# Optimization experiments

Measured on AMD Instinct MI355X. Metric: run time of the kernel, lower is better.

## Reference

```python
import jax, jax.numpy as jnp
import numpy as np

B, H, W, DIM = 16, 64, 64, 256
EXPAND = 2
D_INNER = DIM * EXPAND      # 512
HID = D_INNER // 2          # 256 per GRU direction


def setup_inputs() -> dict:
    ks = jax.random.split(jax.random.key(0), 10)
    g = lambda i, shape, s=0.05: jax.random.normal(ks[i], shape, dtype=jnp.float32) * s
    return {
        "x": jax.random.normal(ks[0], (B, H, W, DIM), dtype=jnp.float32),
        "ln_gamma": jnp.ones((DIM,), jnp.float32),
        "ln_beta": jnp.zeros((DIM,), jnp.float32),
        "mlp_w1": g(1, (32, 4), 0.3),
        "mlp_b1": jnp.zeros((32,), jnp.float32),
        "mlp_w2": g(2, (4, 32), 0.3),
        "mlp_b2": jnp.zeros((4,), jnp.float32),
        "in_w": g(3, (D_INNER, DIM)),
        "in_b": jnp.zeros((D_INNER,), jnp.float32),
        "gru_wih_f": g(4, (3 * HID, D_INNER)),
        "gru_whh_f": g(5, (3 * HID, HID)),
        "gru_bih_f": jnp.zeros((3 * HID,), jnp.float32),
        "gru_bhh_f": jnp.zeros((3 * HID,), jnp.float32),
        "gru_wih_b": g(6, (3 * HID, D_INNER)),
        "gru_whh_b": g(7, (3 * HID, HID)),
        "gru_bih_b": jnp.zeros((3 * HID,), jnp.float32),
        "gru_bhh_b": jnp.zeros((3 * HID,), jnp.float32),
        "out_w": g(8, (DIM, D_INNER)),
        "out_b": jnp.zeros((DIM,), jnp.float32),
    }


def _resize_linear_axis(x, out_size, axis):
    """torch F.interpolate(mode='bilinear', align_corners=False) along one axis
    (the other axis has scale 1 -> identity, so 1-D resize is exact)."""
    in_size = x.shape[axis]
    scale = in_size / out_size
    src = (jnp.arange(out_size, dtype=jnp.float32) + 0.5) * scale - 0.5
    src = jnp.clip(src, 0.0, in_size - 1)
    i0 = jnp.floor(src).astype(jnp.int32)
    i1 = jnp.minimum(i0 + 1, in_size - 1)
    w = (src - i0.astype(jnp.float32))
    x0 = jnp.take(x, i0, axis=axis)
    x1 = jnp.take(x, i1, axis=axis)
    shape = [1] * x.ndim
    shape[axis] = out_size
    w = w.reshape(shape)
    return x0 * (1.0 - w) + x1 * w


def _avgpool3_mean(g):
    """F.avg_pool2d(g, 3, stride=1, padding=1) (count_include_pad=True), then
    spatial mean -> [B, 1]."""
    s = jax.lax.reduce_window(g, 0.0, jax.lax.add, (1, 1, 3, 3), (1, 1, 1, 1),
                              [(0, 0), (0, 0), (1, 1), (1, 1)])
    return (s / 9.0).mean(axis=(2, 3))


def _gru_dir(xp, whh, bhh, reverse):
    """One GRU direction. xp: [B, L, 3h] precomputed input-side gates."""
    hid = whh.shape[1]
    h0 = jnp.zeros((xp.shape[0], hid), xp.dtype)

    def step(h, xt):
        gh = h @ whh.T + bhh
        xr, xz, xn = jnp.split(xt, 3, axis=-1)
        hr, hz, hn = jnp.split(gh, 3, axis=-1)
        r = jax.nn.sigmoid(xr + hr)
        z = jax.nn.sigmoid(xz + hz)
        n = jnp.tanh(xn + r * hn)
        h_new = (1.0 - z) * n + z * h
        return h_new, h_new

    _, ys = jax.lax.scan(step, h0, jnp.swapaxes(xp, 0, 1), reverse=reverse)
    return jnp.swapaxes(ys, 0, 1)  # [B, L, h], ys[t] aligned with input t


def _forward(x, ln_gamma, ln_beta, mlp_w1, mlp_b1, mlp_w2, mlp_b2,
             in_w, in_b, gru_wih_f, gru_whh_f, gru_bih_f, gru_bhh_f,
             gru_wih_b, gru_whh_b, gru_bih_b, gru_bhh_b, out_w, out_b):
    Bx, Hx, Wx, C = x.shape
    # LayerNorm over channels
    mu = x.mean(-1, keepdims=True)
    var = ((x - mu) ** 2).mean(-1, keepdims=True)
    xn = (x - mu) / jnp.sqrt(var + 1e-5) * ln_gamma + ln_beta

    # --- GradientDirectionSelector ---
    gray = xn.mean(-1)[:, None]                                   # [B,1,H,W]
    gp = jnp.pad(gray, ((0, 0), (0, 0), (1, 1), (1, 1)), mode="reflect")
    grad_h = jnp.abs(gp[:, :, :, 2:] - gp[:, :, :, :-2])          # [B,1,H+2,W]
    grad_v = jnp.abs(gp[:, :, 2:, :] - gp[:, :, :-2, :])          # [B,1,H,W+2]
    grad_h = _resize_linear_axis(grad_h, Hx, axis=2)              # [B,1,H,W]
    grad_v = _resize_linear_axis(grad_v, Wx, axis=3)              # [B,1,H,W]
    grad_d = (grad_h + grad_v) * 0.5
    grad_a = jnp.abs(grad_h - grad_v)
    scores = jnp.concatenate(
        [_avgpool3_mean(g) for g in (grad_h, grad_v, grad_d, grad_a)], axis=1)  # [B,4]
    h1 = jax.nn.relu(scores @ mlp_w1.T + mlp_b1)
    logits = h1 @ mlp_w2.T + mlp_b2
    probs = jax.nn.softmax(logits, axis=-1)
    idx = jnp.argmax(probs, axis=-1)  # topk=1 indices, [B]

    # --- direction-routed scan (dir 1 -> vertical transpose; 0/2/3 -> row-major) ---
    seq_h = xn.reshape(Bx, Hx * Wx, C)
    seq_v = jnp.swapaxes(xn, 1, 2).reshape(Bx, Hx * Wx, C)
    seq = jnp.where((idx == 1)[:, None, None], seq_v, seq_h)      # [B,L,C]

    # --- FastSequenceBlock: in_proj -> biGRU -> out_proj ---
    z = seq @ in_w.T + in_b                                       # [B,L,d_inner]
    yf = _gru_dir(z @ gru_wih_f.T + gru_bih_f, gru_whh_f, gru_bhh_f, False)
    yb = _gru_dir(z @ gru_wih_b.T + gru_bih_b, gru_whh_b, gru_bhh_b, True)
    y = jnp.concatenate([yf, yb], axis=-1) @ out_w.T + out_b      # [B,L,C]

    # unscan (row-major reshape, as in the original) + residual
    return x + y.reshape(Bx, Hx, Wx, C)


def reference(x, ln_gamma, ln_beta, mlp_w1, mlp_b1, mlp_w2, mlp_b2,
              in_w, in_b, gru_wih_f, gru_whh_f, gru_bih_f, gru_bhh_f,
              gru_wih_b, gru_whh_b, gru_bih_b, gru_bhh_b, out_w, out_b):
    return _forward(x, ln_gamma, ln_beta, mlp_w1, mlp_b1, mlp_w2, mlp_b2,
                    in_w, in_b, gru_wih_f, gru_whh_f, gru_bih_f, gru_bhh_f,
                    gru_wih_b, gru_whh_b, gru_bih_b, gru_bhh_b, out_w, out_b)
```

## Files before the change

kernel.cpp:

```cpp
#include <hip/hip_runtime.h>


#define L_   4096
#define CH   32
#define NCH  128

typedef __attribute__((ext_vector_type(8))) _Float16 half8;
typedef __attribute__((ext_vector_type(2))) _Float16 half2v;
typedef __attribute__((ext_vector_type(4))) float f32x4;

__device__ __forceinline__ unsigned short f2h(float f) {
  _Float16 h = (_Float16)f;
  return __builtin_bit_cast(unsigned short, h);
}
__device__ __forceinline__ float h2f(unsigned short u) {
  return (float)__builtin_bit_cast(_Float16, u);
}
__device__ __forceinline__ float sigm(float x) {
  return __builtin_amdgcn_rcpf(1.f + __expf(-x));
}
__device__ __forceinline__ float tanhf_(float x) {
  return 1.f - 2.f * __builtin_amdgcn_rcpf(1.f + __expf(2.f * x));
}
__device__ __forceinline__ float dot2(unsigned w, unsigned h, float c) {
  return __builtin_amdgcn_fdot2(__builtin_bit_cast(half2v, w),
                                __builtin_bit_cast(half2v, h), c, false);
}

__global__ __launch_bounds__(256) void k_f2h(const float* __restrict__ in,
                                             unsigned short* __restrict__ out,
                                             int n) {
  int i = blockIdx.x * 256 + threadIdx.x;
  if (i < n) out[i] = f2h(in[i]);
}

__global__ __launch_bounds__(256) void k_wcomb(const float* __restrict__ wih_f,
                                               const float* __restrict__ wih_b,
                                               const float* __restrict__ in_w,
                                               unsigned short* __restrict__ wcomb) {
  const int n = blockIdx.x;
  const float* wrow = (n < 768) ? (wih_f + (long)n * 512)
                                : (wih_b + (long)(n - 768) * 512);
  const int k = threadIdx.x;
  float acc = 0.f;
  for (int j = 0; j < 512; ++j) acc += wrow[j] * in_w[j * 256 + k];
  wcomb[(long)n * 256 + k] = f2h(acc);
}

__global__ __launch_bounds__(256) void k_bcomb(const float* __restrict__ wih_f,
                                               const float* __restrict__ wih_b,
                                               const float* __restrict__ in_b,
                                               const float* __restrict__ bih_f,
                                               const float* __restrict__ bih_b,
                                               const float* __restrict__ bhh_f,
                                               const float* __restrict__ bhh_b,
                                               float* __restrict__ badj) {
  int n = blockIdx.x * 256 + threadIdx.x;
  if (n >= 1536) return;
  const int dir = n >= 768;
  const int g = dir ? (n - 768) : n;
  const float* wrow = (dir ? wih_b : wih_f) + (long)g * 512;
  float acc = (dir ? bih_b : bih_f)[g];
  for (int j = 0; j < 512; ++j) acc += wrow[j] * in_b[j];
  if (g < 512) acc += (dir ? bhh_b : bhh_f)[g];
  badj[n] = acc;
}

__global__ __launch_bounds__(256) void k_ln(const float* __restrict__ x,
                                            const float* __restrict__ gamma,
                                            const float* __restrict__ beta,
                                            unsigned short* __restrict__ xn,
                                            float* __restrict__ gray) {
  const int lane = threadIdx.x & 63;
  const long pix = (long)blockIdx.x * 4 + (threadIdx.x >> 6);
  const float4 v = *(const float4*)(x + pix * 256 + lane * 4);
  float s = v.x + v.y + v.z + v.w;
  float s2 = v.x * v.x + v.y * v.y + v.z * v.z + v.w * v.w;
#pragma unroll
  for (int off = 32; off > 0; off >>= 1) {
    s += __shfl_xor(s, off, 64);
    s2 += __shfl_xor(s2, off, 64);
  }
  const float mu = s * (1.f / 256.f);
  const float var = fmaxf(s2 * (1.f / 256.f) - mu * mu, 0.f);
  const float rstd = rsqrtf(var + 1e-5f);
  const float4 gm = *(const float4*)(gamma + lane * 4);
  const float4 bt = *(const float4*)(beta + lane * 4);
  float o0 = (v.x - mu) * rstd * gm.x + bt.x;
  float o1 = (v.y - mu) * rstd * gm.y + bt.y;
  float o2 = (v.z - mu) * rstd * gm.z + bt.z;
  float o3 = (v.w - mu) * rstd * gm.w + bt.w;
  ushort4 o;
  o.x = f2h(o0); o.y = f2h(o1); o.z = f2h(o2); o.w = f2h(o3);
  *(ushort4*)(xn + pix * 256 + lane * 4) = o;
  float gs = o0 + o1 + o2 + o3;
#pragma unroll
  for (int off = 32; off > 0; off >>= 1) gs += __shfl_xor(gs, off, 64);
  if (lane == 0) gray[pix] = gs * (1.f / 256.f);
}

__device__ __forceinline__ int refl64(int m) {
  return m < 0 ? -m : (m > 63 ? 126 - m : m);
}

__global__ __launch_bounds__(256) void k_sel(const float* __restrict__ gray,
                                             const float* __restrict__ w1,
                                             const float* __restrict__ b1,
                                             const float* __restrict__ w2,
                                             const float* __restrict__ b2,
                                             int* __restrict__ flag) {
  __shared__ float g[64][65];
  __shared__ float part[4][4];
  const int b = blockIdx.x;
  const int tid = threadIdx.x;
  for (int r = 0; r < 16; ++r) {
    int p = tid + 256 * r;
    g[p >> 6][p & 63] = gray[(long)b * 4096 + p];
  }
  __syncthreads();
  const float S = 66.f / 64.f;
  float sh = 0.f, sv = 0.f, sd = 0.f, sa = 0.f;
  for (int rr = 0; rr < 16; ++rr) {
    int p = tid + 256 * rr;
    int h = p >> 6, w = p & 63;
    float srci = (h + 0.5f) * S - 0.5f;
    int i0 = (int)srci;
    float ai = srci - (float)i0;
    int i1 = i0 + 1; if (i1 > 65) i1 = 65;
    int r0 = refl64(i0 - 1), r1 = refl64(i1 - 1);
    int wl = w ? (w - 1) : 1;
    int wr2 = (w == 63) ? 62 : (w + 1);
    float GH0 = fabsf(g[r0][wr2] - g[r0][wl]);
    float GH1 = fabsf(g[r1][wr2] - g[r1][wl]);
    float ghr = GH0 + ai * (GH1 - GH0);
    float srcj = (w + 0.5f) * S - 0.5f;
    int j0 = (int)srcj;
    float aj = srcj - (float)j0;
    int j1 = j0 + 1; if (j1 > 65) j1 = 65;
    int c0 = refl64(j0 - 1), c1 = refl64(j1 - 1);
    int hu = h ? (h - 1) : 1;
    int hd = (h == 63) ? 62 : (h + 1);
    float GV0 = fabsf(g[hd][c0] - g[hu][c0]);
    float GV1 = fabsf(g[hd][c1] - g[hu][c1]);
    float gvr = GV0 + aj * (GV1 - GV0);
    float wt = ((h == 0 || h == 63) ? 2.f : 3.f) *
               ((w == 0 || w == 63) ? 2.f : 3.f);
    sh += wt * ghr;
    sv += wt * gvr;
    sd += wt * 0.5f * (ghr + gvr);
    sa += wt * fabsf(ghr - gvr);
  }
#pragma unroll
  for (int off = 32; off > 0; off >>= 1) {
    sh += __shfl_xor(sh, off, 64);
    sv += __shfl_xor(sv, off, 64);
    sd += __shfl_xor(sd, off, 64);
    sa += __shfl_xor(sa, off, 64);
  }
  if ((tid & 63) == 0) {
    part[tid >> 6][0] = sh; part[tid >> 6][1] = sv;
    part[tid >> 6][2] = sd; part[tid >> 6][3] = sa;
  }
  __syncthreads();
  if (tid == 0) {
    float sc[4];
    for (int k = 0; k < 4; ++k)
      sc[k] = (part[0][k] + part[1][k] + part[2][k] + part[3][k]) * (1.f / 36864.f);
    float logits[4];
    for (int k = 0; k < 4; ++k) logits[k] = b2[k];
    for (int j = 0; j < 32; ++j) {
      float hj = b1[j];
      for (int i = 0; i < 4; ++i) hj += sc[i] * w1[j * 4 + i];
      hj = fmaxf(hj, 0.f);
      for (int k = 0; k < 4; ++k) logits[k] += hj * w2[k * 32 + j];
    }
    int idx = 0;
    float best = logits[0];
    for (int k = 1; k < 4; ++k)
      if (logits[k] > best) { best = logits[k]; idx = k; }
    flag[b] = (idx == 1) ? 1 : 0;
  }
}

__global__ __launch_bounds__(256) void k_gemm(const unsigned short* __restrict__ A,
                                              const unsigned short* __restrict__ Bw,
                                              const float* __restrict__ bias,
                                              const float* __restrict__ resid,
                                              float* __restrict__ out,
                                              int K, int N) {
  __shared__ unsigned short Al[128][40];
  __shared__ unsigned short Bl[128][40];
  const int tid = threadIdx.x;
  const long m0 = (long)blockIdx.x * 128;
  const int n0 = blockIdx.y * 128;
  const int rA = tid >> 2;
  const int cp = (tid & 3) * 8;

  const unsigned short* a0p = A + (m0 + rA) * K + cp;
  const unsigned short* a1p = A + (m0 + rA + 64) * K + cp;
  const unsigned short* b0p = Bw + (long)(n0 + rA) * K + cp;
  const unsigned short* b1p = Bw + (long)(n0 + rA + 64) * K + cp;

  const int wv = tid >> 6, lane = tid & 63;
  const int wm = (wv >> 1) * 64, wn = (wv & 1) * 64;
  const int fr = lane & 15, fq = lane >> 4;

  const f32x4 zero4 = {0.f, 0.f, 0.f, 0.f};
  f32x4 acc[4][4];
#pragma unroll
  for (int i = 0; i < 4; ++i)
#pragma unroll
    for (int j = 0; j < 4; ++j) acc[i][j] = zero4;

  for (int k0 = 0; k0 < K; k0 += 32) {
    half8 va0 = *(const half8*)(a0p + k0);
    half8 va1 = *(const half8*)(a1p + k0);
    half8 vb0 = *(const half8*)(b0p + k0);
    half8 vb1 = *(const half8*)(b1p + k0);
    __syncthreads();
    *(half8*)&Al[rA][cp] = va0;
    *(half8*)&Al[rA + 64][cp] = va1;
    *(half8*)&Bl[rA][cp] = vb0;
    *(half8*)&Bl[rA + 64][cp] = vb1;
    __syncthreads();
    half8 af[4], bf[4];
#pragma unroll
    for (int i = 0; i < 4; ++i) af[i] = *(const half8*)&Al[wm + i * 16 + fr][fq * 8];
#pragma unroll
    for (int j = 0; j < 4; ++j) bf[j] = *(const half8*)&Bl[wn + j * 16 + fr][fq * 8];
#pragma unroll
    for (int i = 0; i < 4; ++i)
#pragma unroll
      for (int j = 0; j < 4; ++j)
        acc[i][j] = __builtin_amdgcn_mfma_f32_16x16x32_f16(af[i], bf[j], acc[i][j], 0, 0, 0);
  }

#pragma unroll
  for (int j = 0; j < 4; ++j) {
    const int col = n0 + wn + j * 16 + fr;
    const float bv = bias[col];
#pragma unroll
    for (int i = 0; i < 4; ++i) {
      const long mbase = m0 + wm + i * 16 + fq * 4;
#pragma unroll
      for (int r = 0; r < 4; ++r) {
        const long m = mbase + r;
        out[m * N + col] = acc[i][j][r] + bv + resid[m * N + col];
      }
    }
  }
}

__global__ __launch_bounds__(768, 3) void k_scan(
    const unsigned short* __restrict__ xn,
    const unsigned short* __restrict__ wcomb,
    const float* __restrict__ badj,
    const unsigned short* __restrict__ whh16,
    const float* __restrict__ bhhf,
    const float* __restrict__ bhhb,
    const int* __restrict__ flag,
    unsigned short* __restrict__ ycat) {
  const int dir = blockIdx.x & 1;
  const int b = blockIdx.x >> 1;
  const unsigned short* whh = whh16 + (long)dir * (768 * 256);
  const float* bhh = dir ? bhhb : bhhf;
  const unsigned short* wcd = wcomb + (long)dir * (768 * 256);
  const float* bcd = badj + dir * 768;
  const int tid = threadIdx.x;
  const int g = tid >> 8;
  const int u = tid & 255;
  const int wv = tid >> 6;
  const int lane = tid & 63;
  const int fr = lane & 15;
  const int fq = lane >> 4;
  const int fb = flag[b];

  __shared__ unsigned short xplds[CH][768];
  __shared__ unsigned short ylds[CH][256];
  __shared__ uint4 hl4[2][32];
  __shared__ float ghlds[512];

  float Bnh = 0.f;
  if (g == 2) Bnh = bhh[512 + u];
  float hreg = 0.f;
  if (tid < 128) ((unsigned*)hl4[0])[tid] = 0;

  const long xnb = (long)b * 4096;
  unsigned short* yb = ycat + (long)b * (L_ * 512) + dir * 256;

  const f32x4 zero4 = {0.f, 0.f, 0.f, 0.f};
  int pb = 0;

  for (int c = 0; c < NCH; ++c) {
    const int cc = dir ? (NCH - 1 - c) : c;
    const int t0 = cc * CH;

    if (c > 0) {
      const int pt0 = (dir ? (NCH - c) : (c - 1)) * CH;
#pragma unroll
      for (int k = 0; k < 2; ++k) {
        const int idx = tid + 768 * k;
        if (idx < 1024) {
          const int tsx = idx >> 5;
          const int cl = (idx & 31) * 8;
          half8 v = *(const half8*)&ylds[tsx][cl];
          *(half8*)(yb + (long)(pt0 + tsx) * 512 + cl) = v;
        }
      }
    }

    {
      const unsigned short* arow0;
      const unsigned short* arow1;
      {
        int t = t0 + fr;
        int p = fb ? (((t & 63) << 6) | (t >> 6)) : t;
        arow0 = xn + (xnb + p) * 256 + fq * 8;
        t = t0 + 16 + fr;
        p = fb ? (((t & 63) << 6) | (t >> 6)) : t;
        arow1 = xn + (xnb + p) * 256 + fq * 8;
      }
      f32x4 acc0[4], acc1[4];
#pragma unroll
      for (int i = 0; i < 4; ++i) { acc0[i] = zero4; acc1[i] = zero4; }
#pragma unroll
      for (int s = 0; s < 8; ++s) {
        half8 a0v = *(const half8*)(arow0 + s * 32);
        half8 a1v = *(const half8*)(arow1 + s * 32);
#pragma unroll
        for (int i = 0; i < 4; ++i) {
          const int n = (wv * 4 + i) * 16 + fr;
          half8 bfr = *(const half8*)(wcd + (long)n * 256 + s * 32 + fq * 8);
          acc0[i] = __builtin_amdgcn_mfma_f32_16x16x32_f16(a0v, bfr, acc0[i], 0, 0, 0);
          acc1[i] = __builtin_amdgcn_mfma_f32_16x16x32_f16(a1v, bfr, acc1[i], 0, 0, 0);
        }
      }
#pragma unroll
      for (int i = 0; i < 4; ++i) {
        const int n = (wv * 4 + i) * 16 + fr;
        const float bv = bcd[n];
#pragma unroll
        for (int r = 0; r < 4; ++r) {
          xplds[fq * 4 + r][n] = f2h(acc0[i][r] + bv);
          xplds[16 + fq * 4 + r][n] = f2h(acc1[i][r] + bv);
        }
      }
    }
    __syncthreads();

    uint4 wq[32];
    {
      const unsigned short* wp = whh + (long)tid * 256;
      asm volatile("" : "+v"(wp));
#pragma unroll
      for (int i = 0; i < 32; ++i) wq[i] = *(const uint4*)(wp + i * 8);
    }

    for (int lt = 0; lt < CH; ++lt) {
      const int ts = dir ? (CH - 1 - lt) : lt;
      const uint4* hp = hl4[pb];
      float a0 = 0.f, a1 = 0.f, a2 = 0.f, a3 = 0.f;
#pragma unroll
      for (int i = 0; i < 32; ++i) {
        uint4 hv = hp[i];
        a0 = dot2(wq[i].x, hv.x, a0);
        a1 = dot2(wq[i].y, hv.y, a1);
        a2 = dot2(wq[i].z, hv.z, a2);
        a3 = dot2(wq[i].w, hv.w, a3);
      }
      const float gh = (a0 + a1) + (a2 + a3);
      if (g == 1) ghlds[u] = h2f(xplds[ts][tid]) + gh;
      else if (g == 2) ghlds[256 + u] = gh + Bnh;
      __syncthreads();
      if (g == 0) {
        const float r = sigm(h2f(xplds[ts][u]) + gh);
        const float z = sigm(ghlds[u]);
        const float n = tanhf_(h2f(xplds[ts][512 + u]) + r * ghlds[256 + u]);
        hreg = n + z * (hreg - n);
        const unsigned short hb = f2h(hreg);
        ((unsigned short*)hl4[pb ^ 1])[u] = hb;
        ylds[ts][u] = hb;
      }
      pb ^= 1;
      __syncthreads();
    }
  }
  {
    const int pt0 = (dir ? 0 : (NCH - 1)) * CH;
#pragma unroll
    for (int k = 0; k < 2; ++k) {
      const int idx = tid + 768 * k;
      if (idx < 1024) {
        const int tsx = idx >> 5;
        const int cl = (idx & 31) * 8;
        half8 v = *(const half8*)&ylds[tsx][cl];
        *(half8*)(yb + (long)(pt0 + tsx) * 512 + cl) = v;
      }
    }
  }
}

extern "C" void kernel_launch(void* const* d_in, const int* in_sizes, int n_in,
                              void* d_out, int out_size, void* d_ws, size_t ws_size,
                              hipStream_t stream) {
  (void)in_sizes; (void)n_in; (void)out_size; (void)ws_size;
  const float* x     = (const float*)d_in[0];
  const float* lng   = (const float*)d_in[1];
  const float* lnb   = (const float*)d_in[2];
  const float* w1    = (const float*)d_in[3];
  const float* b1    = (const float*)d_in[4];
  const float* w2    = (const float*)d_in[5];
  const float* b2    = (const float*)d_in[6];
  const float* in_w  = (const float*)d_in[7];
  const float* in_b  = (const float*)d_in[8];
  const float* wih_f = (const float*)d_in[9];
  const float* whh_f = (const float*)d_in[10];
  const float* bih_f = (const float*)d_in[11];
  const float* bhh_f = (const float*)d_in[12];
  const float* wih_b = (const float*)d_in[13];
  const float* whh_b = (const float*)d_in[14];
  const float* bih_b = (const float*)d_in[15];
  const float* bhh_b = (const float*)d_in[16];
  const float* out_w = (const float*)d_in[17];
  const float* out_b = (const float*)d_in[18];

  char* ws = (char*)d_ws;
  unsigned short* xn     = (unsigned short*)(ws + 0);
  float*          gray   = (float*)(ws + 33554432);
  int*            flag   = (int*)(ws + 33816576);
  unsigned short* whh16  = (unsigned short*)(ws + 33816832);
  unsigned short* outw16 = (unsigned short*)(ws + 34603264);
  unsigned short* wcomb  = (unsigned short*)(ws + 34865408);
  float*          badj   = (float*)(ws + 35651840);
  unsigned short* ycat   = (unsigned short*)(ws + 35658240);

  k_f2h<<<768, 256, 0, stream>>>(whh_f, whh16, 196608);
  k_f2h<<<768, 256, 0, stream>>>(whh_b, whh16 + 196608, 196608);
  k_f2h<<<512, 256, 0, stream>>>(out_w, outw16, 131072);
  k_wcomb<<<1536, 256, 0, stream>>>(wih_f, wih_b, in_w, wcomb);
  k_bcomb<<<6, 256, 0, stream>>>(wih_f, wih_b, in_b, bih_f, bih_b,
                                 bhh_f, bhh_b, badj);
  k_ln<<<16384, 256, 0, stream>>>(x, lng, lnb, xn, gray);
  k_sel<<<16, 256, 0, stream>>>(gray, w1, b1, w2, b2, flag);
  k_scan<<<32, 768, 0, stream>>>(xn, wcomb, badj, whh16,
                                 bhh_f, bhh_b, flag, ycat);
  dim3 gout(512, 2);
  k_gemm<<<gout, 256, 0, stream>>>(ycat, outw16, out_b, x, (float*)d_out, 512, 256);
}
```

Measured before the change: 8.337 ms.

## Collapse GRU scan to 256 threads computing all three gates per unit

The recurrent scan block shrinks from 768 to 256 threads, and each thread now computes the r, z and n hidden dot products for one unit. The r-gate weights stay pinned in registers once for the whole kernel, while the z and n weights are re-read from a new interleaved global layout (built by a new repack kernel) on every timestep. This removes one of the two block barriers per step and the LDS exchange of gate partial sums. The cost is three times the dot-product work per thread on each serial step, plus heavy global or L2 weight traffic inside the latency-bound loop.

```diff
diff --git a/kernel.cpp b/kernel.cpp
--- a/kernel.cpp
+++ b/kernel.cpp
@@ -8,6 +8,7 @@
 typedef __attribute__((ext_vector_type(8))) _Float16 half8;
 typedef __attribute__((ext_vector_type(2))) _Float16 half2v;
 typedef __attribute__((ext_vector_type(4))) float f32x4;
+typedef __attribute__((ext_vector_type(4))) unsigned uvec4;
 
 __device__ __forceinline__ unsigned short f2h(float f) {
   _Float16 h = (_Float16)f;
@@ -32,6 +33,27 @@
                                              int n) {
   int i = blockIdx.x * 256 + threadIdx.x;
   if (i < n) out[i] = f2h(in[i]);
+}
+
+__global__ __launch_bounds__(256) void k_whhS(const float* __restrict__ whh_f,
+                                              const float* __restrict__ whh_b,
+                                              uvec4* __restrict__ whhS) {
+  const int blk = blockIdx.x;
+  const int dir = blk / 96;
+  const int rem = blk - dir * 96;
+  const int gate = rem >> 5;
+  const int kblk = rem & 31;
+  const int t = threadIdx.x;
+  const float* src = (dir ? whh_b : whh_f) + (long)(gate * 256 + t) * 256 + kblk * 8;
+  unsigned short h[8];
+#pragma unroll
+  for (int j = 0; j < 8; ++j) h[j] = f2h(src[j]);
+  uvec4 v;
+  v.x = (unsigned)h[0] | ((unsigned)h[1] << 16);
+  v.y = (unsigned)h[2] | ((unsigned)h[3] << 16);
+  v.z = (unsigned)h[4] | ((unsigned)h[5] << 16);
+  v.w = (unsigned)h[6] | ((unsigned)h[7] << 16);
+  whhS[(long)blk * 256 + t] = v;
 }
 
 __global__ __launch_bounds__(256) void k_wcomb(const float* __restrict__ wih_f,
@@ -251,24 +273,22 @@
   }
 }
 
-__global__ __launch_bounds__(768, 3) void k_scan(
+__global__ __launch_bounds__(256, 1) void k_scan(
     const unsigned short* __restrict__ xn,
     const unsigned short* __restrict__ wcomb,
     const float* __restrict__ badj,
-    const unsigned short* __restrict__ whh16,
+    const uvec4* __restrict__ whhS,
     const float* __restrict__ bhhf,
     const float* __restrict__ bhhb,
     const int* __restrict__ flag,
     unsigned short* __restrict__ ycat) {
   const int dir = blockIdx.x & 1;
   const int b = blockIdx.x >> 1;
-  const unsigned short* whh = whh16 + (long)dir * (768 * 256);
+  const uvec4* wS = whhS + (long)dir * (3 * 32 * 256);
   const float* bhh = dir ? bhhb : bhhf;
   const unsigned short* wcd = wcomb + (long)dir * (768 * 256);
   const float* bcd = badj + dir * 768;
   const int tid = threadIdx.x;
-  const int g = tid >> 8;
-  const int u = tid & 255;
   const int wv = tid >> 6;
   const int lane = tid & 63;
   const int fr = lane & 15;
@@ -277,13 +297,34 @@
 
   __shared__ unsigned short xplds[CH][768];
   __shared__ unsigned short ylds[CH][256];
-  __shared__ uint4 hl4[2][32];
-  __shared__ float ghlds[512];
-
-  float Bnh = 0.f;
-  if (g == 2) Bnh = bhh[512 + u];
+  __shared__ uvec4 hl4[2][32];
+
+  const float Bnh = bhh[512 + tid];
   float hreg = 0.f;
   if (tid < 128) ((unsigned*)hl4[0])[tid] = 0;
+
+  const uvec4* rp = wS + tid;
+  uvec4 w00 = rp[0 * 256],  w01 = rp[1 * 256],  w02 = rp[2 * 256],  w03 = rp[3 * 256];
+  uvec4 w04 = rp[4 * 256],  w05 = rp[5 * 256],  w06 = rp[6 * 256],  w07 = rp[7 * 256];
+  uvec4 w08 = rp[8 * 256],  w09 = rp[9 * 256],  w10 = rp[10 * 256], w11 = rp[11 * 256];
+  uvec4 w12 = rp[12 * 256], w13 = rp[13 * 256], w14 = rp[14 * 256], w15 = rp[15 * 256];
+  uvec4 w16 = rp[16 * 256], w17 = rp[17 * 256], w18 = rp[18 * 256], w19 = rp[19 * 256];
+  uvec4 w20 = rp[20 * 256], w21 = rp[21 * 256], w22 = rp[22 * 256], w23 = rp[23 * 256];
+  uvec4 w24 = rp[24 * 256], w25 = rp[25 * 256], w26 = rp[26 * 256], w27 = rp[27 * 256];
+  uvec4 w28 = rp[28 * 256], w29 = rp[29 * 256], w30 = rp[30 * 256], w31 = rp[31 * 256];
+  asm volatile("" : "+v"(w00), "+v"(w01), "+v"(w02), "+v"(w03),
+                    "+v"(w04), "+v"(w05), "+v"(w06), "+v"(w07));
+  asm volatile("" : "+v"(w08), "+v"(w09), "+v"(w10), "+v"(w11),
+                    "+v"(w12), "+v"(w13), "+v"(w14), "+v"(w15));
+  asm volatile("" : "+v"(w16), "+v"(w17), "+v"(w18), "+v"(w19),
+                    "+v"(w20), "+v"(w21), "+v"(w22), "+v"(w23));
+  asm volatile("" : "+v"(w24), "+v"(w25), "+v"(w26), "+v"(w27),
+                    "+v"(w28), "+v"(w29), "+v"(w30), "+v"(w31));
+
+  const uvec4* zp = wS + 32 * 256 + tid;
+  const uvec4* np = wS + 64 * 256 + tid;
+
+  __syncthreads();
 
   const long xnb = (long)b * 4096;
   unsigned short* yb = ycat + (long)b * (L_ * 512) + dir * 256;
@@ -298,14 +339,12 @@
     if (c > 0) {
       const int pt0 = (dir ? (NCH - c) : (c - 1)) * CH;
 #pragma unroll
-      for (int k = 0; k < 2; ++k) {
-        const int idx = tid + 768 * k;
-        if (idx < 1024) {
-          const int tsx = idx >> 5;
-          const int cl = (idx & 31) * 8;
-          half8 v = *(const half8*)&ylds[tsx][cl];
-          *(half8*)(yb + (long)(pt0 + tsx) * 512 + cl) = v;
-        }
+      for (int k = 0; k < 4; ++k) {
+        const int idx = tid + 256 * k;
+        const int tsx = idx >> 5;
+        const int cl = (idx & 31) * 8;
+        half8 v = *(const half8*)&ylds[tsx][cl];
+        *(half8*)(yb + (long)(pt0 + tsx) * 512 + cl) = v;
       }
     }
 
@@ -320,67 +359,83 @@
         p = fb ? (((t & 63) << 6) | (t >> 6)) : t;
         arow1 = xn + (xnb + p) * 256 + fq * 8;
       }
-      f32x4 acc0[4], acc1[4];
-#pragma unroll
-      for (int i = 0; i < 4; ++i) { acc0[i] = zero4; acc1[i] = zero4; }
-#pragma unroll
-      for (int s = 0; s < 8; ++s) {
-        half8 a0v = *(const half8*)(arow0 + s * 32);
-        half8 a1v = *(const half8*)(arow1 + s * 32);
-#pragma unroll
-        for (int i = 0; i < 4; ++i) {
-          const int n = (wv * 4 + i) * 16 + fr;
-          half8 bfr = *(const half8*)(wcd + (long)n * 256 + s * 32 + fq * 8);
-          acc0[i] = __builtin_amdgcn_mfma_f32_16x16x32_f16(a0v, bfr, acc0[i], 0, 0, 0);
-          acc1[i] = __builtin_amdgcn_mfma_f32_16x16x32_f16(a1v, bfr, acc1[i], 0, 0, 0);
+#pragma unroll
+      for (int hf = 0; hf < 4; ++hf) {
+        f32x4 acc0[3], acc1[3];
+#pragma unroll
+        for (int j = 0; j < 3; ++j) { acc0[j] = zero4; acc1[j] = zero4; }
+#pragma unroll
+        for (int s = 0; s < 8; ++s) {
+          half8 a0v = *(const half8*)(arow0 + s * 32);
+          half8 a1v = *(const half8*)(arow1 + s * 32);
+#pragma unroll
+          for (int j = 0; j < 3; ++j) {
+            const int n = wv * 192 + hf * 48 + j * 16 + fr;
+            half8 bfr = *(const half8*)(wcd + (long)n * 256 + s * 32 + fq * 8);
+            acc0[j] = __builtin_amdgcn_mfma_f32_16x16x32_f16(a0v, bfr, acc0[j], 0, 0, 0);
+            acc1[j] = __builtin_amdgcn_mfma_f32_16x16x32_f16(a1v, bfr, acc1[j], 0, 0, 0);
+          }
         }
-      }
-#pragma unroll
-      for (int i = 0; i < 4; ++i) {
-        const int n = (wv * 4 + i) * 16 + fr;
-        const float bv = bcd[n];
-#pragma unroll
-        for (int r = 0; r < 4; ++r) {
-          xplds[fq * 4 + r][n] = f2h(acc0[i][r] + bv);
-          xplds[16 + fq * 4 + r][n] = f2h(acc1[i][r] + bv);
+#pragma unroll
+        for (int j = 0; j < 3; ++j) {
+          const int n = wv * 192 + hf * 48 + j * 16 + fr;
+          const float bv = bcd[n];
+#pragma unroll
+          for (int r = 0; r < 4; ++r) {
+            xplds[fq * 4 + r][n] = f2h(acc0[j][r] + bv);
+            xplds[16 + fq * 4 + r][n] = f2h(acc1[j][r] + bv);
+          }
         }
       }
     }
     __syncthreads();
 
-    uint4 wq[32];
-    {
-      const unsigned short* wp = whh + (long)tid * 256;
-      asm volatile("" : "+v"(wp));
-#pragma unroll
-      for (int i = 0; i < 32; ++i) wq[i] = *(const uint4*)(wp + i * 8);
-    }
-
     for (int lt = 0; lt < CH; ++lt) {
       const int ts = dir ? (CH - 1 - lt) : lt;
-      const uint4* hp = hl4[pb];
-      float a0 = 0.f, a1 = 0.f, a2 = 0.f, a3 = 0.f;
-#pragma unroll
-      for (int i = 0; i < 32; ++i) {
-        uint4 hv = hp[i];
-        a0 = dot2(wq[i].x, hv.x, a0);
-        a1 = dot2(wq[i].y, hv.y, a1);
-        a2 = dot2(wq[i].z, hv.z, a2);
-        a3 = dot2(wq[i].w, hv.w, a3);
+      const float xr = h2f(xplds[ts][tid]);
+      const float xz = h2f(xplds[ts][256 + tid]);
+      const float xnv = h2f(xplds[ts][512 + tid]);
+      const uvec4* hp = hl4[pb];
+      float ar0 = 0.f, ar1 = 0.f, ar2 = 0.f, ar3 = 0.f;
+      float az0 = 0.f, az1 = 0.f, az2 = 0.f, az3 = 0.f;
+      float an0 = 0.f, an1 = 0.f, an2 = 0.f, an3 = 0.f;
+#define STEP_I(I, W)                                   \
+      {                                                \
+        uvec4 hv = hp[I];                              \
+        uvec4 zq = zp[(I) * 256];                      \
+        uvec4 nq = np[(I) * 256];                      \
+        ar0 = dot2(W.x, hv.x, ar0);                    \
+        ar1 = dot2(W.y, hv.y, ar1);                    \
+        ar2 = dot2(W.z, hv.z, ar2);                    \
+        ar3 = dot2(W.w, hv.w, ar3);                    \
+        az0 = dot2(zq.x, hv.x, az0);                   \
+        az1 = dot2(zq.y, hv.y, az1);                   \
+        az2 = dot2(zq.z, hv.z, az2);                   \
+        az3 = dot2(zq.w, hv.w, az3);                   \
+        an0 = dot2(nq.x, hv.x, an0);                   \
+        an1 = dot2(nq.y, hv.y, an1);                   \
+        an2 = dot2(nq.z, hv.z, an2);                   \
+        an3 = dot2(nq.w, hv.w, an3);                   \
       }
-      const float gh = (a0 + a1) + (a2 + a3);
-      if (g == 1) ghlds[u] = h2f(xplds[ts][tid]) + gh;
-      else if (g == 2) ghlds[256 + u] = gh + Bnh;
-      __syncthreads();
-      if (g == 0) {
-        const float r = sigm(h2f(xplds[ts][u]) + gh);
-        const float z = sigm(ghlds[u]);
-        const float n = tanhf_(h2f(xplds[ts][512 + u]) + r * ghlds[256 + u]);
-        hreg = n + z * (hreg - n);
-        const unsigned short hb = f2h(hreg);
-        ((unsigned short*)hl4[pb ^ 1])[u] = hb;
-        ylds[ts][u] = hb;
-      }
+      STEP_I(0, w00)  STEP_I(1, w01)  STEP_I(2, w02)  STEP_I(3, w03)
+      STEP_I(4, w04)  STEP_I(5, w05)  STEP_I(6, w06)  STEP_I(7, w07)
+      STEP_I(8, w08)  STEP_I(9, w09)  STEP_I(10, w10) STEP_I(11, w11)
+      STEP_I(12, w12) STEP_I(13, w13) STEP_I(14, w14) STEP_I(15, w15)
+      STEP_I(16, w16) STEP_I(17, w17) STEP_I(18, w18) STEP_I(19, w19)
+      STEP_I(20, w20) STEP_I(21, w21) STEP_I(22, w22) STEP_I(23, w23)
+      STEP_I(24, w24) STEP_I(25, w25) STEP_I(26, w26) STEP_I(27, w27)
+      STEP_I(28, w28) STEP_I(29, w29) STEP_I(30, w30) STEP_I(31, w31)
+#undef STEP_I
+      const float ghr = (ar0 + ar1) + (ar2 + ar3);
+      const float ghz = (az0 + az1) + (az2 + az3);
+      const float ghn = (an0 + an1) + (an2 + an3);
+      const float r = sigm(xr + ghr);
+      const float z = sigm(xz + ghz);
+      const float n = tanhf_(xnv + r * (ghn + Bnh));
+      hreg = n + z * (hreg - n);
+      const unsigned short hb = f2h(hreg);
+      ((unsigned short*)hl4[pb ^ 1])[tid] = hb;
+      ylds[ts][tid] = hb;
       pb ^= 1;
       __syncthreads();
     }
@@ -388,14 +443,12 @@
   {
     const int pt0 = (dir ? 0 : (NCH - 1)) * CH;
 #pragma unroll
-    for (int k = 0; k < 2; ++k) {
-      const int idx = tid + 768 * k;
-      if (idx < 1024) {
-        const int tsx = idx >> 5;
-        const int cl = (idx & 31) * 8;
-        half8 v = *(const half8*)&ylds[tsx][cl];
-        *(half8*)(yb + (long)(pt0 + tsx) * 512 + cl) = v;
-      }
+    for (int k = 0; k < 4; ++k) {
+      const int idx = tid + 256 * k;
+      const int tsx = idx >> 5;
+      const int cl = (idx & 31) * 8;
+      half8 v = *(const half8*)&ylds[tsx][cl];
+      *(half8*)(yb + (long)(pt0 + tsx) * 512 + cl) = v;
     }
   }
 }
@@ -428,21 +481,20 @@
   unsigned short* xn     = (unsigned short*)(ws + 0);
   float*          gray   = (float*)(ws + 33554432);
   int*            flag   = (int*)(ws + 33816576);
-  unsigned short* whh16  = (unsigned short*)(ws + 33816832);
+  uvec4*          whhS   = (uvec4*)(ws + 33816832);
   unsigned short* outw16 = (unsigned short*)(ws + 34603264);
   unsigned short* wcomb  = (unsigned short*)(ws + 34865408);
   float*          badj   = (float*)(ws + 35651840);
   unsigned short* ycat   = (unsigned short*)(ws + 35658240);
 
-  k_f2h<<<768, 256, 0, stream>>>(whh_f, whh16, 196608);
-  k_f2h<<<768, 256, 0, stream>>>(whh_b, whh16 + 196608, 196608);
+  k_whhS<<<192, 256, 0, stream>>>(whh_f, whh_b, whhS);
   k_f2h<<<512, 256, 0, stream>>>(out_w, outw16, 131072);
   k_wcomb<<<1536, 256, 0, stream>>>(wih_f, wih_b, in_w, wcomb);
   k_bcomb<<<6, 256, 0, stream>>>(wih_f, wih_b, in_b, bih_f, bih_b,
                                  bhh_f, bhh_b, badj);
   k_ln<<<16384, 256, 0, stream>>>(x, lng, lnb, xn, gray);
   k_sel<<<16, 256, 0, stream>>>(gray, w1, b1, w2, b2, flag);
-  k_scan<<<32, 768, 0, stream>>>(xn, wcomb, badj, whh16,
+  k_scan<<<32, 256, 0, stream>>>(xn, wcomb, badj, whhS,
                                  bhh_f, bhh_b, flag, ycat);
   dim3 gout(512, 2);
   k_gemm<<<gout, 256, 0, stream>>>(ycat, outw16, out_b, x, (float*)d_out, 512, 256);
```

Result: slower. 10.63 ms (+27.5%).

## Split GRU recurrent weights across registers, LDS and streamed global; K-split scan

Applied to the files above, without the earlier changes.

The scan kernel moves from 768 threads (one gate row per thread) to 512 threads, where each thread computes all three gates for one hidden unit over half of the K dimension. The two halves are combined through an LDS partial-sum buffer. Recurrent weights are pre-packed by a new k_pack kernel into three tiers: 20 vectors kept in registers, 14 kept in LDS, and 14 re-streamed from global every step. The goal is to keep the weight working set on-chip and to cut the per-step gate exchange. The chunk size drops to 16 timesteps, so the input-projection MFMA runs more often on smaller tiles. The trade-off is that every step now depends on global-load latency for the streamed tier.

```diff
diff --git a/kernel.cpp b/kernel.cpp
--- a/kernel.cpp
+++ b/kernel.cpp
@@ -2,12 +2,13 @@
 
 
 #define L_   4096
-#define CH   32
-#define NCH  128
+#define CH   16
+#define NCH  256
 
 typedef __attribute__((ext_vector_type(8))) _Float16 half8;
 typedef __attribute__((ext_vector_type(2))) _Float16 half2v;
 typedef __attribute__((ext_vector_type(4))) float f32x4;
+typedef __attribute__((ext_vector_type(4))) unsigned uvec4;
 
 __device__ __forceinline__ unsigned short f2h(float f) {
   _Float16 h = (_Float16)f;
@@ -32,6 +33,32 @@
                                              int n) {
   int i = blockIdx.x * 256 + threadIdx.x;
   if (i < n) out[i] = f2h(in[i]);
+}
+
+__global__ __launch_bounds__(64) void k_pack(const float* __restrict__ whh_f,
+                                             const float* __restrict__ whh_b,
+                                             uvec4* __restrict__ whhREG,
+                                             uvec4* __restrict__ whhLDSg,
+                                             uvec4* __restrict__ whhSTR) {
+  const int dt = blockIdx.x;
+  const int d = dt >> 9;
+  const int t = dt & 511;
+  const int p = t >> 8, u = t & 255;
+  const int j = threadIdx.x;
+  if (j >= 48) return;
+  const int gate = j >> 4, jj = j & 15;
+  const float* src = (d ? whh_b : whh_f) + (long)(gate * 256 + u) * 256 + p * 128 + jj * 8;
+  unsigned short h[8];
+#pragma unroll
+  for (int q = 0; q < 8; ++q) h[q] = f2h(src[q]);
+  uvec4 v;
+  v.x = (unsigned)h[0] | ((unsigned)h[1] << 16);
+  v.y = (unsigned)h[2] | ((unsigned)h[3] << 16);
+  v.z = (unsigned)h[4] | ((unsigned)h[5] << 16);
+  v.w = (unsigned)h[6] | ((unsigned)h[7] << 16);
+  if (j < 20)      whhREG[(long)dt * 20 + j] = v;
+  else if (j < 34) whhLDSg[(long)(d * 14 + (j - 20)) * 512 + t] = v;
+  else             whhSTR[(long)dt * 14 + (j - 34)] = v;
 }
 
 __global__ __launch_bounds__(256) void k_wcomb(const float* __restrict__ wih_f,
@@ -251,42 +278,51 @@
   }
 }
 
-__global__ __launch_bounds__(768, 3) void k_scan(
+__global__ __launch_bounds__(512, 1) void k_scan(
     const unsigned short* __restrict__ xn,
     const unsigned short* __restrict__ wcomb,
     const float* __restrict__ badj,
-    const unsigned short* __restrict__ whh16,
+    const uvec4* __restrict__ whhREG,
+    const uvec4* __restrict__ whhLDSg,
+    const uvec4* __restrict__ whhSTR,
     const float* __restrict__ bhhf,
     const float* __restrict__ bhhb,
     const int* __restrict__ flag,
     unsigned short* __restrict__ ycat) {
   const int dir = blockIdx.x & 1;
   const int b = blockIdx.x >> 1;
-  const unsigned short* whh = whh16 + (long)dir * (768 * 256);
   const float* bhh = dir ? bhhb : bhhf;
   const unsigned short* wcd = wcomb + (long)dir * (768 * 256);
   const float* bcd = badj + dir * 768;
   const int tid = threadIdx.x;
-  const int g = tid >> 8;
-  const int u = tid & 255;
   const int wv = tid >> 6;
   const int lane = tid & 63;
   const int fr = lane & 15;
   const int fq = lane >> 4;
+  const int p = tid >> 8;
+  const int u = tid & 255;
   const int fb = flag[b];
 
   __shared__ unsigned short xplds[CH][768];
   __shared__ unsigned short ylds[CH][256];
-  __shared__ uint4 hl4[2][32];
-  __shared__ float ghlds[512];
-
-  float Bnh = 0.f;
-  if (g == 2) Bnh = bhh[512 + u];
+  __shared__ uvec4 wlds[14][512];
+  __shared__ uvec4 hl4[2][32];
+  __shared__ float part[256][5];
+
+  {
+    const uvec4* src = whhLDSg + (long)dir * (14 * 512);
+#pragma unroll
+    for (int i = 0; i < 14; ++i) wlds[i][tid] = src[i * 512 + tid];
+  }
+  const float Bnh = (p == 0) ? bhh[512 + u] : 0.f;
   float hreg = 0.f;
   if (tid < 128) ((unsigned*)hl4[0])[tid] = 0;
+  __syncthreads();
 
   const long xnb = (long)b * 4096;
   unsigned short* yb = ycat + (long)b * (L_ * 512) + dir * 256;
+  const uvec4* regp = whhREG + (long)(dir * 512 + tid) * 20;
+  const uvec4* strp0 = whhSTR + (long)(dir * 512 + tid) * 14;
 
   const f32x4 zero4 = {0.f, 0.f, 0.f, 0.f};
   int pb = 0;
@@ -297,85 +333,120 @@
 
     if (c > 0) {
       const int pt0 = (dir ? (NCH - c) : (c - 1)) * CH;
-#pragma unroll
-      for (int k = 0; k < 2; ++k) {
-        const int idx = tid + 768 * k;
-        if (idx < 1024) {
-          const int tsx = idx >> 5;
-          const int cl = (idx & 31) * 8;
-          half8 v = *(const half8*)&ylds[tsx][cl];
-          *(half8*)(yb + (long)(pt0 + tsx) * 512 + cl) = v;
-        }
-      }
+      const int tsx = tid >> 5;
+      const int cl = (tid & 31) * 8;
+      half8 v = *(const half8*)&ylds[tsx][cl];
+      *(half8*)(yb + (long)(pt0 + tsx) * 512 + cl) = v;
     }
 
     {
       const unsigned short* arow0;
-      const unsigned short* arow1;
       {
         int t = t0 + fr;
-        int p = fb ? (((t & 63) << 6) | (t >> 6)) : t;
-        arow0 = xn + (xnb + p) * 256 + fq * 8;
-        t = t0 + 16 + fr;
-        p = fb ? (((t & 63) << 6) | (t >> 6)) : t;
-        arow1 = xn + (xnb + p) * 256 + fq * 8;
+        int pp = fb ? (((t & 63) << 6) | (t >> 6)) : t;
+        arow0 = xn + (xnb + pp) * 256 + fq * 8;
       }
-      f32x4 acc0[4], acc1[4];
-#pragma unroll
-      for (int i = 0; i < 4; ++i) { acc0[i] = zero4; acc1[i] = zero4; }
-#pragma unroll
-      for (int s = 0; s < 8; ++s) {
-        half8 a0v = *(const half8*)(arow0 + s * 32);
-        half8 a1v = *(const half8*)(arow1 + s * 32);
-#pragma unroll
-        for (int i = 0; i < 4; ++i) {
-          const int n = (wv * 4 + i) * 16 + fr;
-          half8 bfr = *(const half8*)(wcd + (long)n * 256 + s * 32 + fq * 8);
-          acc0[i] = __builtin_amdgcn_mfma_f32_16x16x32_f16(a0v, bfr, acc0[i], 0, 0, 0);
-          acc1[i] = __builtin_amdgcn_mfma_f32_16x16x32_f16(a1v, bfr, acc1[i], 0, 0, 0);
+#pragma unroll
+      for (int hf = 0; hf < 2; ++hf) {
+        f32x4 acc0[3];
+#pragma unroll
+        for (int i = 0; i < 3; ++i) acc0[i] = zero4;
+#pragma unroll
+        for (int s = 0; s < 8; ++s) {
+          half8 a0v = *(const half8*)(arow0 + s * 32);
+#pragma unroll
+          for (int i = 0; i < 3; ++i) {
+            const int jj = hf * 3 + i;
+            const int n = (jj >> 1) * 256 + wv * 32 + (jj & 1) * 16 + fr;
+            half8 bfr = *(const half8*)(wcd + (long)n * 256 + s * 32 + fq * 8);
+            acc0[i] = __builtin_amdgcn_mfma_f32_16x16x32_f16(a0v, bfr, acc0[i], 0, 0, 0);
+          }
         }
-      }
-#pragma unroll
-      for (int i = 0; i < 4; ++i) {
-        const int n = (wv * 4 + i) * 16 + fr;
-        const float bv = bcd[n];
-#pragma unroll
-        for (int r = 0; r < 4; ++r) {
-          xplds[fq * 4 + r][n] = f2h(acc0[i][r] + bv);
-          xplds[16 + fq * 4 + r][n] = f2h(acc1[i][r] + bv);
+#pragma unroll
+        for (int i = 0; i < 3; ++i) {
+          const int jj = hf * 3 + i;
+          const int n = (jj >> 1) * 256 + wv * 32 + (jj & 1) * 16 + fr;
+          const float bv = bcd[n];
+#pragma unroll
+          for (int r = 0; r < 4; ++r)
+            xplds[fq * 4 + r][n] = f2h(acc0[i][r] + bv);
         }
       }
     }
     __syncthreads();
 
-    uint4 wq[32];
-    {
-      const unsigned short* wp = whh + (long)tid * 256;
-      asm volatile("" : "+v"(wp));
-#pragma unroll
-      for (int i = 0; i < 32; ++i) wq[i] = *(const uint4*)(wp + i * 8);
-    }
+    const uvec4* rp2 = regp;
+    asm volatile("" : "+v"(rp2));
+    uvec4 r00 = rp2[0],  r01 = rp2[1],  r02 = rp2[2],  r03 = rp2[3];
+    uvec4 r04 = rp2[4],  r05 = rp2[5],  r06 = rp2[6],  r07 = rp2[7];
+    uvec4 r08 = rp2[8],  r09 = rp2[9],  r10 = rp2[10], r11 = rp2[11];
+    uvec4 r12 = rp2[12], r13 = rp2[13], r14 = rp2[14], r15 = rp2[15];
+    uvec4 r16 = rp2[16], r17 = rp2[17], r18 = rp2[18], r19 = rp2[19];
+    asm volatile("" : "+v"(r00), "+v"(r01), "+v"(r02), "+v"(r03),
+                      "+v"(r04), "+v"(r05), "+v"(r06), "+v"(r07));
+    asm volatile("" : "+v"(r08), "+v"(r09), "+v"(r10), "+v"(r11),
+                      "+v"(r12), "+v"(r13), "+v"(r14), "+v"(r15));
+    asm volatile("" : "+v"(r16), "+v"(r17), "+v"(r18), "+v"(r19));
 
     for (int lt = 0; lt < CH; ++lt) {
       const int ts = dir ? (CH - 1 - lt) : lt;
-      const uint4* hp = hl4[pb];
-      float a0 = 0.f, a1 = 0.f, a2 = 0.f, a3 = 0.f;
-#pragma unroll
-      for (int i = 0; i < 32; ++i) {
-        uint4 hv = hp[i];
-        a0 = dot2(wq[i].x, hv.x, a0);
-        a1 = dot2(wq[i].y, hv.y, a1);
-        a2 = dot2(wq[i].z, hv.z, a2);
-        a3 = dot2(wq[i].w, hv.w, a3);
+      const uvec4* sp = strp0;
+      asm volatile("" : "+v"(sp));
+      int wb = 0;
+      asm volatile("" : "+v"(wb));
+      const uvec4* hp = &hl4[pb][p * 16];
+      float ar0 = 0.f, ar1 = 0.f, az0 = 0.f, az1 = 0.f, an0 = 0.f, an1 = 0.f;
+#define JSTEP(J, WR, ZEXPR, NEXPR)                       \
+      {                                                  \
+        uvec4 hv = hp[J];                                \
+        uvec4 wz = (ZEXPR);                              \
+        uvec4 wn = (NEXPR);                              \
+        ar0 = dot2(WR.x, hv.x, ar0);                     \
+        ar1 = dot2(WR.y, hv.y, ar1);                     \
+        ar0 = dot2(WR.z, hv.z, ar0);                     \
+        ar1 = dot2(WR.w, hv.w, ar1);                     \
+        az0 = dot2(wz.x, hv.x, az0);                     \
+        az1 = dot2(wz.y, hv.y, az1);                     \
+        az0 = dot2(wz.z, hv.z, az0);                     \
+        az1 = dot2(wz.w, hv.w, az1);                     \
+        an0 = dot2(wn.x, hv.x, an0);                     \
+        an1 = dot2(wn.y, hv.y, an1);                     \
+        an0 = dot2(wn.z, hv.z, an0);                     \
+        an1 = dot2(wn.w, hv.w, an1);                     \
       }
-      const float gh = (a0 + a1) + (a2 + a3);
-      if (g == 1) ghlds[u] = h2f(xplds[ts][tid]) + gh;
-      else if (g == 2) ghlds[256 + u] = gh + Bnh;
+      JSTEP(0,  r00, r16,               wlds[wb + 12][tid])
+      JSTEP(1,  r01, r17,               wlds[wb + 13][tid])
+      JSTEP(2,  r02, r18,               sp[0])
+      JSTEP(3,  r03, r19,               sp[1])
+      JSTEP(4,  r04, wlds[wb + 0][tid], sp[2])
+      JSTEP(5,  r05, wlds[wb + 1][tid], sp[3])
+      JSTEP(6,  r06, wlds[wb + 2][tid], sp[4])
+      JSTEP(7,  r07, wlds[wb + 3][tid], sp[5])
+      JSTEP(8,  r08, wlds[wb + 4][tid], sp[6])
+      JSTEP(9,  r09, wlds[wb + 5][tid], sp[7])
+      JSTEP(10, r10, wlds[wb + 6][tid], sp[8])
+      JSTEP(11, r11, wlds[wb + 7][tid], sp[9])
+      JSTEP(12, r12, wlds[wb + 8][tid], sp[10])
+      JSTEP(13, r13, wlds[wb + 9][tid], sp[11])
+      JSTEP(14, r14, wlds[wb + 10][tid], sp[12])
+      JSTEP(15, r15, wlds[wb + 11][tid], sp[13])
+#undef JSTEP
+      if (p == 1) {
+        part[u][0] = ar0 + ar1;
+        part[u][1] = az0 + az1;
+        part[u][2] = an0 + an1;
+      }
       __syncthreads();
-      if (g == 0) {
-        const float r = sigm(h2f(xplds[ts][u]) + gh);
-        const float z = sigm(ghlds[u]);
-        const float n = tanhf_(h2f(xplds[ts][512 + u]) + r * ghlds[256 + u]);
+      if (p == 0) {
+        const float xr = h2f(xplds[ts][u]);
+        const float xz = h2f(xplds[ts][256 + u]);
+        const float xnv = h2f(xplds[ts][512 + u]);
+        const float ghr = ar0 + ar1 + part[u][0];
+        const float ghz = az0 + az1 + part[u][1];
+        const float ghn = an0 + an1 + part[u][2];
+        const float r = sigm(xr + ghr);
+        const float z = sigm(xz + ghz);
+        const float n = tanhf_(xnv + r * (ghn + Bnh));
         hreg = n + z * (hreg - n);
         const unsigned short hb = f2h(hreg);
         ((unsigned short*)hl4[pb ^ 1])[u] = hb;
@@ -387,16 +458,10 @@
   }
   {
     const int pt0 = (dir ? 0 : (NCH - 1)) * CH;
-#pragma unroll
-    for (int k = 0; k < 2; ++k) {
-      const int idx = tid + 768 * k;
-      if (idx < 1024) {
-        const int tsx = idx >> 5;
-        const int cl = (idx & 31) * 8;
-        half8 v = *(const half8*)&ylds[tsx][cl];
-        *(half8*)(yb + (long)(pt0 + tsx) * 512 + cl) = v;
-      }
-    }
+    const int tsx = tid >> 5;
+    const int cl = (tid & 31) * 8;
+    half8 v = *(const half8*)&ylds[tsx][cl];
+    *(half8*)(yb + (long)(pt0 + tsx) * 512 + cl) = v;
   }
 }
 
@@ -428,21 +493,22 @@
   unsigned short* xn     = (unsigned short*)(ws + 0);
   float*          gray   = (float*)(ws + 33554432);
   int*            flag   = (int*)(ws + 33816576);
-  unsigned short* whh16  = (unsigned short*)(ws + 33816832);
+  uvec4*          whhREG = (uvec4*)(ws + 33816832);
+  uvec4*          whhLDSg= (uvec4*)(ws + 34144512);
+  uvec4*          whhSTR = (uvec4*)(ws + 34373888);
   unsigned short* outw16 = (unsigned short*)(ws + 34603264);
   unsigned short* wcomb  = (unsigned short*)(ws + 34865408);
   float*          badj   = (float*)(ws + 35651840);
   unsigned short* ycat   = (unsigned short*)(ws + 35658240);
 
-  k_f2h<<<768, 256, 0, stream>>>(whh_f, whh16, 196608);
-  k_f2h<<<768, 256, 0, stream>>>(whh_b, whh16 + 196608, 196608);
+  k_pack<<<1024, 64, 0, stream>>>(whh_f, whh_b, whhREG, whhLDSg, whhSTR);
   k_f2h<<<512, 256, 0, stream>>>(out_w, outw16, 131072);
   k_wcomb<<<1536, 256, 0, stream>>>(wih_f, wih_b, in_w, wcomb);
   k_bcomb<<<6, 256, 0, stream>>>(wih_f, wih_b, in_b, bih_f, bih_b,
                                  bhh_f, bhh_b, badj);
   k_ln<<<16384, 256, 0, stream>>>(x, lng, lnb, xn, gray);
   k_sel<<<16, 256, 0, stream>>>(gray, w1, b1, w2, b2, flag);
-  k_scan<<<32, 768, 0, stream>>>(xn, wcomb, badj, whh16,
+  k_scan<<<32, 512, 0, stream>>>(xn, wcomb, badj, whhREG, whhLDSg, whhSTR,
                                  bhh_f, bhh_b, flag, ycat);
   dim3 gout(512, 2);
   k_gemm<<<gout, 256, 0, stream>>>(ycat, outw16, out_b, x, (float*)d_out, 512, 256);
```

Measured after the change: 17.11 ms. 2.05x slower.
